# Kernel optimization log

Measured on AMD Instinct MI355X. Metric: run time of the kernel, lower is better.

## Reference

```python
import jax, jax.numpy as jnp
import numpy as np

NODE, PROJ, ATTN, NREL, NL = 1280, 2560, 256, 129, 4
B, L = 2, 1024
EPS = 1e-5


def _layernorm(x):
    m = jnp.mean(x, axis=-1, keepdims=True)
    v = jnp.var(x, axis=-1, keepdims=True)
    return (x - m) * jax.lax.rsqrt(v + EPS)


def _rope(x):
    # x: [B, L, 2, D]; rotary applied along the seq (L) axis, rotate-half convention
    d = x.shape[-1]
    freq = 10000.0 ** (-jnp.arange(0, d, 2, dtype=jnp.float32) / d)      # [d/2]
    ang = jnp.arange(x.shape[1], dtype=jnp.float32)[:, None] * freq      # [L, d/2]
    cos = jnp.concatenate([jnp.cos(ang), jnp.cos(ang)], -1)[:, None, :]  # [L,1,d]
    sin = jnp.concatenate([jnp.sin(ang), jnp.sin(ang)], -1)[:, None, :]
    x1, x2 = jnp.split(x, 2, axis=-1)
    return x * cos + jnp.concatenate([-x2, x1], -1) * sin


def _relpos_idx(n):
    i = np.arange(n)
    one = NREL // 2
    return jnp.asarray(np.clip(i[:, None] - i[None, :], -one, one) + one)  # [L,L] int32


def setup_inputs() -> dict:
    key = jax.random.key(0)
    ks = jax.random.split(key, 14)
    s = 0.02
    return {
        "node": jax.random.normal(ks[0], (B, L, NODE), jnp.float32),
        "qk_scaling": jax.random.uniform(ks[1], (B, L, 1), jnp.float32),
        "bias": jax.random.normal(ks[2], (B, 1, L), jnp.float32),
        "cond": jax.random.normal(ks[3], (B, NODE), jnp.float32),
        "w_gva": jax.random.normal(ks[4], (NL, NODE, 2 * PROJ + ATTN), jnp.float32) * s,
        "b_gva": jnp.zeros((NL, 2 * PROJ + ATTN), jnp.float32),
        "mhs_w": jax.random.normal(ks[5], (NL, 2, ATTN), jnp.float32) * s + 1.0,
        "mhs_b": jax.random.normal(ks[6], (NL, 2, ATTN), jnp.float32) * s,
        "relpos_emb": jax.random.normal(ks[7], (NL, NREL), jnp.float32) * s,
        "w_out": jax.random.normal(ks[8], (NL, PROJ, NODE), jnp.float32) * s,
        "b_out": jnp.zeros((NL, NODE), jnp.float32),
        "w_adaln": jax.random.normal(ks[9], (NL, NODE, 3 * NODE), jnp.float32) * s,
        "b_adaln": jnp.zeros((NL, 3 * NODE), jnp.float32),
        "subbatch_size": 256,
    }


def _forward(node, qk_scaling, bias, cond, w_gva, b_gva, mhs_w, mhs_b,
             relpos_emb, w_out, b_out, w_adaln, b_adaln, rel_idx):
    edge = None
    silu = jax.nn.silu
    for l in range(NL):
        # AdaLN conditioning: SiLU -> Linear(node, 3*node), chunk into gamma/beta/alpha [B,node]
        gba = silu(cond) @ w_adaln[l] + b_adaln[l]
        gamma, beta, alpha = jnp.split(gba, 3, axis=-1)
        shortcut = node
        x = _layernorm(node)
        x = x * (1.0 + gamma[:, None, :]) + beta[:, None, :]
        # GAU: joint gate/value/base projection + SiLU
        h = silu(x @ w_gva[l] + b_gva[l])                    # [B,L,2P+A]
        gates = h[..., :PROJ]
        values = h[..., PROJ:2 * PROJ]
        base = h[..., 2 * PROJ:]                             # [B,L,A]
        # multi-headed scaling (2 heads) + RoPE, unbind into q,k
        qk = base[..., None, :] * mhs_w[l] + mhs_b[l]        # [B,L,2,A]
        qk = _rope(qk)
        q, k = qk[..., 0, :], qk[..., 1, :]
        # attention with mask bias + relpos bias; query pre-scaled
        rel = relpos_emb[l][rel_idx]                         # [L,L]
        logits = jnp.einsum('bid,bjd->bij', q * qk_scaling, k) + (bias + rel)
        attn = jax.nn.softmax(logits, axis=-1)               # [B,L,L]
        out = jnp.einsum('bij,bjd->bid', attn, values)       # [B,L,P]
        edge = jnp.sum(attn, axis=-3)                        # sum-reduce over batch -> [L,L]
        out = out * gates
        out = out @ w_out[l] + b_out[l]
        node = out * (1.0 + alpha[:, None, :]) + shortcut
    return node, edge


def reference(node, qk_scaling, bias, cond, w_gva, b_gva, mhs_w, mhs_b,
              relpos_emb, w_out, b_out, w_adaln, b_adaln, subbatch_size):
    # subbatch_size only chunks queries for memory in the original; math-identical ignored
    rel_idx = _relpos_idx(node.shape[-2])
    return _forward(node, qk_scaling, bias, cond, w_gva, b_gva, mhs_w, mhs_b,
                    relpos_emb, w_out, b_out, w_adaln, b_adaln, rel_idx)
```

## Files before the change

### kernel.cpp

```cpp
#include <hip/hip_runtime.h>


typedef __bf16 bf16;
typedef __attribute__((ext_vector_type(8))) __bf16 bf16x8;
typedef __attribute__((ext_vector_type(4))) float f32x4;

#define NODE_D 1280
#define PROJ_D 2560
#define ATTN_D 256
#define HDIM 5376
#define LSEQ 1024
#define NTOK 2048

__device__ __forceinline__ void async_ld16(const void* gsrc, void* ldst) {
  __builtin_amdgcn_global_load_lds(
      (__attribute__((address_space(1))) void*)gsrc,
      (__attribute__((address_space(3))) void*)ldst, 16, 0, 0);
}

__device__ __forceinline__ float sigmoidf_fast(float x) {
  return 1.f / (1.f + __expf(-x));
}

template <int MODE>
__global__ __launch_bounds__(256, 3) void gemm_bt(
    const bf16* __restrict__ A, const bf16* __restrict__ Bt, int K,
    int lda, int ldb, void* __restrict__ C, int ldc,
    const void* __restrict__ E0, const void* __restrict__ E1,
    long zA, long zB, long zCb, long zE0b) {
  __shared__ __align__(16) bf16 As[128 * 64];
  __shared__ __align__(16) bf16 Bs[128 * 64];

  const int z = blockIdx.z;
  A += (size_t)zA * z;
  Bt += (size_t)zB * z;
  char* Cb = (char*)C + (size_t)zCb * z;
  const char* e0 = (const char*)E0 + (size_t)zE0b * z;

  const int rowBase = blockIdx.y * 128;
  const int colBase = blockIdx.x * 128;
  const int tid = threadIdx.x;
  const int lane = tid & 63;
  const int wv = tid >> 6;
  const int wrow = (wv >> 1) * 64;
  const int wcol = (wv & 1) * 64;
  const int fm = lane & 15;
  const int fq = lane >> 4;

  const bf16* Ablk = A + (size_t)rowBase * lda;
  const bf16* Bblk = Bt + (size_t)colBase * ldb;

  f32x4 zero = {0.f, 0.f, 0.f, 0.f};
  f32x4 acc[4][4];
#pragma unroll
  for (int i = 0; i < 4; i++)
#pragma unroll
    for (int j = 0; j < 4; j++) acc[i][j] = zero;

  for (int k0 = 0; k0 < K; k0 += 64) {
    __syncthreads();
#pragma unroll
    for (int i = 0; i < 4; i++) {
      const int slot = tid + i * 256;
      const int row = slot >> 3;
      const int u = (slot & 7) ^ (row & 7);
      bf16* dA = As + ((i * 256 + wv * 64) << 3);
      bf16* dB = Bs + ((i * 256 + wv * 64) << 3);
      async_ld16(Ablk + (size_t)row * lda + k0 + (u << 3), dA);
      async_ld16(Bblk + (size_t)row * ldb + k0 + (u << 3), dB);
    }
    __syncthreads();

#pragma unroll
    for (int s = 0; s < 2; s++) {
      bf16x8 aF[4], bF[4];
#pragma unroll
      for (int i = 0; i < 4; i++) {
        const int r = wrow + i * 16 + fm;
        aF[i] = *(const bf16x8*)(As + r * 64 +
                                 ((((s << 2) | fq) ^ (r & 7)) << 3));
      }
#pragma unroll
      for (int j = 0; j < 4; j++) {
        const int r = wcol + j * 16 + fm;
        bF[j] = *(const bf16x8*)(Bs + r * 64 +
                                 ((((s << 2) | fq) ^ (r & 7)) << 3));
      }
#pragma unroll
      for (int i = 0; i < 4; i++)
#pragma unroll
        for (int j = 0; j < 4; j++)
          acc[i][j] = __builtin_amdgcn_mfma_f32_16x16x32_bf16(
              aF[i], bF[j], acc[i][j], 0, 0, 0);
    }
  }

#pragma unroll
  for (int i = 0; i < 4; i++) {
#pragma unroll
    for (int t = 0; t < 4; t++) {
      const int r = rowBase + wrow + i * 16 + fq * 4 + t;
#pragma unroll
      for (int j = 0; j < 4; j++) {
        const int cc = colBase + wcol + j * 16 + fm;
        float v = acc[i][j][t];
        if constexpr (MODE == 0) {
          v += ((const float*)e0)[cc];
          v = v * sigmoidf_fast(v);
          ((bf16*)Cb)[(size_t)r * ldc + cc] = (bf16)v;
        } else if constexpr (MODE == 1) {
          v += ((const float*)e0)[cc];
          int d = r - cc;
          d = d < -64 ? -64 : (d > 64 ? 64 : d);
          v += ((const float*)E1)[d + 64];
          ((float*)Cb)[(size_t)r * ldc + cc] = v;
        } else if constexpr (MODE == 2) {
          float gt = (float)((const bf16*)e0)[(size_t)r * HDIM + cc];
          ((bf16*)Cb)[(size_t)r * ldc + cc] = (bf16)(v * gt);
        } else {
          ((float*)Cb)[(size_t)r * ldc + cc] = v;
        }
      }
    }
  }
}

__global__ void transpose_f2b(const float* __restrict__ in, bf16* __restrict__ out,
                              int ldin, int ldout) {
  __shared__ __align__(16) bf16 t[64][72];
  const int rb = blockIdx.y * 64, cb = blockIdx.x * 64;
  const int tx = threadIdx.x & 7, ty = threadIdx.x >> 3;
#pragma unroll
  for (int rr = 0; rr < 64; rr += 32) {
    const int r = ty + rr;
    const float4* p = (const float4*)&in[(size_t)(rb + r) * ldin + cb + tx * 8];
    float4 a = p[0], b = p[1];
    t[tx * 8 + 0][r] = (bf16)a.x; t[tx * 8 + 1][r] = (bf16)a.y;
    t[tx * 8 + 2][r] = (bf16)a.z; t[tx * 8 + 3][r] = (bf16)a.w;
    t[tx * 8 + 4][r] = (bf16)b.x; t[tx * 8 + 5][r] = (bf16)b.y;
    t[tx * 8 + 6][r] = (bf16)b.z; t[tx * 8 + 7][r] = (bf16)b.w;
  }
  __syncthreads();
#pragma unroll
  for (int rr = 0; rr < 64; rr += 32) {
    const int c = ty + rr;
    *(bf16x8*)&out[(size_t)(cb + c) * ldout + rb + tx * 8] =
        *(const bf16x8*)&t[c][tx * 8];
  }
}

__global__ void transpose_int(const bf16* __restrict__ in0, bf16* __restrict__ out0,
                              int ldin, int ldout, long zIn, long zOut) {
  __shared__ __align__(16) bf16 t[64][72];
  const bf16* in = in0 + (size_t)zIn * blockIdx.z;
  bf16* out = out0 + (size_t)zOut * blockIdx.z;
  const int rb = blockIdx.y * 64, cb = blockIdx.x * 64;
  const int tx = threadIdx.x & 7, ty = threadIdx.x >> 3;
#pragma unroll
  for (int rr = 0; rr < 64; rr += 32) {
    const int r = ty + rr;
    bf16x8 v = *(const bf16x8*)&in[(size_t)(rb + r) * ldin + cb + tx * 8];
#pragma unroll
    for (int e = 0; e < 8; e++) t[tx * 8 + e][r] = v[e];
  }
  __syncthreads();
#pragma unroll
  for (int rr = 0; rr < 64; rr += 32) {
    const int c = ty + rr;
    *(bf16x8*)&out[(size_t)(cb + c) * ldout + rb + tx * 8] =
        *(const bf16x8*)&t[c][tx * 8];
  }
}

__global__ void gba_init(const float* __restrict__ b_adaln,
                         float* __restrict__ gba) {
  const int i = blockIdx.x * 256 + threadIdx.x;
  if (i < 4 * 2 * 3840) {
    const int l = i / (2 * 3840);
    const int c = i % 3840;
    gba[i] = b_adaln[l * 3840 + c];
  }
}

__global__ void adaln_part(const float* __restrict__ cond,
                           const float* __restrict__ w_adaln,
                           float* __restrict__ gba) {
  __shared__ float sc[2 * NODE_D];
  __shared__ float red[2][2][128];
  const int l = blockIdx.y, z = blockIdx.z;
  const int cl = threadIdx.x & 127;
  const int col = blockIdx.x * 128 + cl;
  const int kg = threadIdx.x >> 7;
  for (int i = threadIdx.x; i < 2 * NODE_D; i += 256) {
    float v = cond[i];
    sc[i] = v * sigmoidf_fast(v);
  }
  __syncthreads();
  const float* w = w_adaln + (size_t)l * NODE_D * 3840;
  const int k0 = z * 160 + kg * 80;
  float a0 = 0.f, a1 = 0.f;
  for (int k = k0; k < k0 + 80; k++) {
    float wv = w[(size_t)k * 3840 + col];
    a0 += sc[k] * wv;
    a1 += sc[NODE_D + k] * wv;
  }
  red[kg][0][cl] = a0;
  red[kg][1][cl] = a1;
  __syncthreads();
  if (kg == 0) {
    a0 += red[1][0][cl];
    a1 += red[1][1][cl];
    atomicAdd(&gba[(size_t)(l * 2 + 0) * 3840 + col], a0);
    atomicAdd(&gba[(size_t)(l * 2 + 1) * 3840 + col], a1);
  }
}

__global__ void ln_mod_kernel(const float* __restrict__ nodef,
                              const float* __restrict__ gba_l,
                              bf16* __restrict__ xmod) {
  __shared__ float red[2][4];
  const int row = blockIdx.x, b = row >> 10, tt = threadIdx.x;
  const float* x = nodef + (size_t)row * NODE_D;
  float vals[5], s = 0.f, s2 = 0.f;
#pragma unroll
  for (int i = 0; i < 5; i++) {
    float v = x[tt + i * 256];
    vals[i] = v; s += v; s2 += v * v;
  }
#pragma unroll
  for (int off = 32; off >= 1; off >>= 1) {
    s += __shfl_down(s, off, 64);
    s2 += __shfl_down(s2, off, 64);
  }
  const int wv = tt >> 6, lane = tt & 63;
  if (lane == 0) { red[0][wv] = s; red[1][wv] = s2; }
  __syncthreads();
  s = red[0][0] + red[0][1] + red[0][2] + red[0][3];
  s2 = red[1][0] + red[1][1] + red[1][2] + red[1][3];
  const float mean = s * (1.f / NODE_D);
  const float var = s2 * (1.f / NODE_D) - mean * mean;
  const float inv = rsqrtf(var + 1e-5f);
  const float* gm = gba_l + b * 3840;
#pragma unroll
  for (int i = 0; i < 5; i++) {
    const int c = tt + i * 256;
    float v = (vals[i] - mean) * inv * (1.f + gm[c]) + gm[NODE_D + c];
    xmod[(size_t)row * NODE_D + c] = (bf16)v;
  }
}

template <bool LAST>
__global__ void res_ln_fuse(const float* __restrict__ p0,
                            const float* __restrict__ p1,
                            const float* __restrict__ b_out_l,
                            const float* __restrict__ gba_l,
                            const float* __restrict__ gba_next,
                            float* __restrict__ nodef,
                            bf16* __restrict__ xmod,
                            float* __restrict__ outNode) {
  __shared__ float red[2][4];
  const int row = blockIdx.x, b = row >> 10, tt = threadIdx.x;
  const float* a0 = p0 + (size_t)row * NODE_D;
  const float* a1 = p1 + (size_t)row * NODE_D;
  float* nd = nodef + (size_t)row * NODE_D;
  const float* al = gba_l + b * 3840 + 2560;
  float vals[5], s = 0.f, s2 = 0.f;
#pragma unroll
  for (int i = 0; i < 5; i++) {
    const int c = tt + i * 256;
    float delta = (a0[c] + a1[c] + b_out_l[c]) * (1.f + al[c]);
    float v = nd[c] + delta;
    if (LAST) {
      outNode[(size_t)row * NODE_D + c] = v;
    } else {
      nd[c] = v;
    }
    vals[i] = v; s += v; s2 += v * v;
  }
  if (!LAST) {
#pragma unroll
    for (int off = 32; off >= 1; off >>= 1) {
      s += __shfl_down(s, off, 64);
      s2 += __shfl_down(s2, off, 64);
    }
    const int wv = tt >> 6, lane = tt & 63;
    if (lane == 0) { red[0][wv] = s; red[1][wv] = s2; }
    __syncthreads();
    s = red[0][0] + red[0][1] + red[0][2] + red[0][3];
    s2 = red[1][0] + red[1][1] + red[1][2] + red[1][3];
    const float mean = s * (1.f / NODE_D);
    const float var = s2 * (1.f / NODE_D) - mean * mean;
    const float inv = rsqrtf(var + 1e-5f);
    const float* gm = gba_next + b * 3840;
#pragma unroll
    for (int i = 0; i < 5; i++) {
      const int c = tt + i * 256;
      float v = (vals[i] - mean) * inv * (1.f + gm[c]) + gm[NODE_D + c];
      xmod[(size_t)row * NODE_D + c] = (bf16)v;
    }
  }
}

__global__ void trig_init(float* __restrict__ tab) {
  const int pos = blockIdx.x;
  const int j = threadIdx.x;
  const float freq = __expf(-(float)j * 0.07195578415606392f);
  const float ang = (float)pos * freq;
  tab[(pos * 128 + j) * 2 + 0] = cosf(ang);
  tab[(pos * 128 + j) * 2 + 1] = sinf(ang);
}

__global__ void qk_rope_kernel(const bf16* __restrict__ h,
                               const float* __restrict__ mhs_w,
                               const float* __restrict__ mhs_b,
                               const float* __restrict__ qk_sc,
                               const float* __restrict__ trig,
                               bf16* __restrict__ q, bf16* __restrict__ k) {
  const int tok = blockIdx.x;
  const int pos = tok & (LSEQ - 1);
  const int d = threadIdx.x;
  const bf16* base = h + (size_t)tok * HDIM + 2 * PROJ_D;
  const int j = d & 127;
  const float2 cssn = ((const float2*)trig)[pos * 128 + j];
  const float cs = cssn.x, sn = cssn.y;
  const float bd = (float)base[d];
  const int pd = (d < 128) ? d + 128 : d - 128;
  const float bp = (float)base[pd];
  const float sgn = (d < 128) ? -1.f : 1.f;

  float v = bd * mhs_w[d] + mhs_b[d];
  float vp = bp * mhs_w[pd] + mhs_b[pd];
  float r0 = v * cs + sgn * vp * sn;
  q[(size_t)tok * ATTN_D + d] = (bf16)(r0 * qk_sc[tok]);

  float v1 = bd * mhs_w[ATTN_D + d] + mhs_b[ATTN_D + d];
  float v1p = bp * mhs_w[ATTN_D + pd] + mhs_b[ATTN_D + pd];
  float r1 = v1 * cs + sgn * v1p * sn;
  k[(size_t)tok * ATTN_D + d] = (bf16)r1;
}

__global__ void softmax_kernel(const float* __restrict__ S, bf16* __restrict__ P) {
  __shared__ float red[8];
  const size_t row = blockIdx.x;
  const float* s = S + row * LSEQ;
  const int tt = threadIdx.x, wv = tt >> 6, lane = tt & 63;
  float v[4];
  float m = -1e30f;
#pragma unroll
  for (int i = 0; i < 4; i++) {
    v[i] = s[tt + i * 256];
    m = fmaxf(m, v[i]);
  }
#pragma unroll
  for (int off = 32; off >= 1; off >>= 1) m = fmaxf(m, __shfl_down(m, off, 64));
  if (lane == 0) red[wv] = m;
  __syncthreads();
  m = fmaxf(fmaxf(red[0], red[1]), fmaxf(red[2], red[3]));
  float sum = 0.f;
#pragma unroll
  for (int i = 0; i < 4; i++) {
    v[i] = __expf(v[i] - m);
    sum += v[i];
  }
#pragma unroll
  for (int off = 32; off >= 1; off >>= 1) sum += __shfl_down(sum, off, 64);
  __syncthreads();
  if (lane == 0) red[4 + wv] = sum;
  __syncthreads();
  const float inv = 1.f / (red[4] + red[5] + red[6] + red[7]);
  bf16* p = P + row * LSEQ;
#pragma unroll
  for (int i = 0; i < 4; i++) p[tt + i * 256] = (bf16)(v[i] * inv);
}

__global__ void copy_f32(const float* __restrict__ in, float* __restrict__ out,
                         int n) {
  int i = (blockIdx.x * 256 + threadIdx.x) * 4;
  if (i < n) *(float4*)(out + i) = *(const float4*)(in + i);
}

__global__ void edge_kernel(const bf16* __restrict__ P, float* __restrict__ out) {
  const int idx = (blockIdx.x * 256 + threadIdx.x) * 4;
#pragma unroll
  for (int i = 0; i < 4; i++)
    out[idx + i] = (float)P[idx + i] + (float)P[1048576 + idx + i];
}

extern "C" void kernel_launch(void* const* d_in, const int* in_sizes, int n_in,
                              void* d_out, int out_size, void* d_ws, size_t ws_size,
                              hipStream_t stream) {
  const float* node_in = (const float*)d_in[0];
  const float* qk_sc   = (const float*)d_in[1];
  const float* bias    = (const float*)d_in[2];
  const float* cond    = (const float*)d_in[3];
  const float* w_gva   = (const float*)d_in[4];
  const float* b_gva   = (const float*)d_in[5];
  const float* mhs_w   = (const float*)d_in[6];
  const float* mhs_b   = (const float*)d_in[7];
  const float* relpos  = (const float*)d_in[8];
  const float* w_out   = (const float*)d_in[9];
  const float* b_out   = (const float*)d_in[10];
  const float* w_adaln = (const float*)d_in[11];
  const float* b_adaln = (const float*)d_in[12];
  (void)in_sizes; (void)n_in; (void)out_size; (void)ws_size;

  char* wsp = (char*)d_ws;
  auto alloc = [&](size_t bytes) {
    char* p = wsp;
    wsp += (bytes + 255) & ~(size_t)255;
    return p;
  };
  float* nodef = (float*)alloc((size_t)NTOK * NODE_D * 4);
  float* gba   = (float*)alloc((size_t)8 * 3840 * 4);
  bf16* xmod   = (bf16*)alloc((size_t)NTOK * NODE_D * 2);
  bf16* h      = (bf16*)alloc((size_t)NTOK * HDIM * 2);
  bf16* q      = (bf16*)alloc((size_t)NTOK * ATTN_D * 2);
  bf16* kk     = (bf16*)alloc((size_t)NTOK * ATTN_D * 2);
  bf16* Vt     = (bf16*)alloc((size_t)2 * PROJ_D * LSEQ * 2);
  bf16* wT     = (bf16*)alloc((size_t)HDIM * NODE_D * 2);
  float* S     = (float*)wT;
  bf16* P      = (bf16*)alloc((size_t)2 * LSEQ * LSEQ * 2);
  bf16* po     = (bf16*)alloc((size_t)NTOK * PROJ_D * 2);
  float* Pp    = (float*)alloc((size_t)2 * NTOK * NODE_D * 4);
  float* trig  = (float*)alloc((size_t)LSEQ * 128 * 2 * 4);

  float* outNode = (float*)d_out;
  float* outEdge = outNode + (size_t)NTOK * NODE_D;

  copy_f32<<<2560, 256, 0, stream>>>(node_in, nodef, NTOK * NODE_D);
  trig_init<<<1024, 128, 0, stream>>>(trig);
  gba_init<<<120, 256, 0, stream>>>(b_adaln, gba);
  adaln_part<<<dim3(30, 4, 8), 256, 0, stream>>>(cond, w_adaln, gba);
  ln_mod_kernel<<<2048, 256, 0, stream>>>(nodef, gba, xmod);

  for (int l = 0; l < 4; ++l) {
    transpose_f2b<<<dim3(84, 20), 256, 0, stream>>>(
        w_gva + (size_t)l * NODE_D * HDIM, wT, HDIM, NODE_D);
    gemm_bt<0><<<dim3(42, 16, 1), 256, 0, stream>>>(
        xmod, wT, NODE_D, NODE_D, NODE_D, h, HDIM,
        b_gva + (size_t)l * HDIM, nullptr, 0, 0, 0, 0);

    qk_rope_kernel<<<2048, 256, 0, stream>>>(h, mhs_w + l * 2 * ATTN_D,
                                             mhs_b + l * 2 * ATTN_D, qk_sc,
                                             trig, q, kk);

    transpose_int<<<dim3(40, 16, 2), 256, 0, stream>>>(
        h + PROJ_D, Vt, HDIM, LSEQ, (long)LSEQ * HDIM, (long)PROJ_D * LSEQ);

    gemm_bt<1><<<dim3(8, 8, 2), 256, 0, stream>>>(
        q, kk, ATTN_D, ATTN_D, ATTN_D, S, LSEQ,
        bias, relpos + l * 129,
        (long)LSEQ * ATTN_D, (long)LSEQ * ATTN_D, (long)LSEQ * LSEQ * 4,
        (long)LSEQ * 4);

    softmax_kernel<<<2048, 256, 0, stream>>>(S, P);
    if (l == 3) edge_kernel<<<1024, 256, 0, stream>>>(P, outEdge);

    gemm_bt<2><<<dim3(20, 8, 2), 256, 0, stream>>>(
        P, Vt, LSEQ, LSEQ, LSEQ, po, PROJ_D,
        h, nullptr,
        (long)LSEQ * LSEQ, (long)PROJ_D * LSEQ, (long)LSEQ * PROJ_D * 2,
        (long)LSEQ * HDIM * 2);

    transpose_f2b<<<dim3(20, 40), 256, 0, stream>>>(
        w_out + (size_t)l * PROJ_D * NODE_D, wT, NODE_D, PROJ_D);
    gemm_bt<4><<<dim3(10, 16, 2), 256, 0, stream>>>(
        po, wT, 1280, PROJ_D, PROJ_D, Pp, NODE_D,
        nullptr, nullptr,
        1280, 1280, (long)NTOK * NODE_D * 4, 0);

    if (l < 3) {
      res_ln_fuse<false><<<2048, 256, 0, stream>>>(
          Pp, Pp + (size_t)NTOK * NODE_D, b_out + (size_t)l * NODE_D,
          gba + l * 2 * 3840, gba + (l + 1) * 2 * 3840, nodef, xmod, nullptr);
    } else {
      res_ln_fuse<true><<<2048, 256, 0, stream>>>(
          Pp, Pp + (size_t)NTOK * NODE_D, b_out + (size_t)l * NODE_D,
          gba + l * 2 * 3840, nullptr, nodef, nullptr, outNode);
    }
  }
}
```

Before: 793.6 us.

## Batch weight transposes upfront, drop node copy, and swizzle GEMM block order

All four layers' w_gva and w_out transposes are batched into two launches before the layer loop, with a dedicated buffer per layer, and S gets its own allocation instead of aliasing the weight buffer. The initial node copy kernel is removed: the first LN and the first residual read node_in directly. The GEMM also remaps block indices into eight interleaved groups to change L2 locality across workgroups. This trades more workspace memory for fewer launches and a different block-to-tile mapping.

After: 811.1 us. +2.2%, slower.

```diff
diff --git a/kernel.cpp b/kernel.cpp
--- a/kernel.cpp
+++ b/kernel.cpp
@@ -37,8 +37,21 @@
   char* Cb = (char*)C + (size_t)zCb * z;
   const char* e0 = (const char*)E0 + (size_t)zE0b * z;
 
-  const int rowBase = blockIdx.y * 128;
-  const int colBase = blockIdx.x * 128;
+  int bx = blockIdx.x, by = blockIdx.y;
+  {
+    const int gx = gridDim.x, gy = gridDim.y;
+    const int n = gx * gy;
+    if ((n & 7) == 0) {
+      const int cpx = n >> 3;
+      const int p = by * gx + bx;
+      const int lg = (p & 7) * cpx + (p >> 3);
+      bx = lg / gy;
+      by = lg % gy;
+    }
+  }
+
+  const int rowBase = by * 128;
+  const int colBase = bx * 128;
   const int tid = threadIdx.x;
   const int lane = tid & 63;
   const int wv = tid >> 6;
@@ -125,9 +138,12 @@
   }
 }
 
-__global__ void transpose_f2b(const float* __restrict__ in, bf16* __restrict__ out,
-                              int ldin, int ldout) {
+__global__ void transpose_f2b(const float* __restrict__ in0,
+                              bf16* __restrict__ out0, int ldin, int ldout,
+                              long zIn, long zOut) {
   __shared__ __align__(16) bf16 t[64][72];
+  const float* in = in0 + (size_t)zIn * blockIdx.z;
+  bf16* out = out0 + (size_t)zOut * blockIdx.z;
   const int rb = blockIdx.y * 64, cb = blockIdx.x * 64;
   const int tx = threadIdx.x & 7, ty = threadIdx.x >> 3;
 #pragma unroll
@@ -215,12 +231,12 @@
   }
 }
 
-__global__ void ln_mod_kernel(const float* __restrict__ nodef,
+__global__ void ln_mod_kernel(const float* __restrict__ xin,
                               const float* __restrict__ gba_l,
                               bf16* __restrict__ xmod) {
   __shared__ float red[2][4];
   const int row = blockIdx.x, b = row >> 10, tt = threadIdx.x;
-  const float* x = nodef + (size_t)row * NODE_D;
+  const float* x = xin + (size_t)row * NODE_D;
   float vals[5], s = 0.f, s2 = 0.f;
 #pragma unroll
   for (int i = 0; i < 5; i++) {
@@ -255,6 +271,7 @@
                             const float* __restrict__ b_out_l,
                             const float* __restrict__ gba_l,
                             const float* __restrict__ gba_next,
+                            const float* __restrict__ resid,
                             float* __restrict__ nodef,
                             bf16* __restrict__ xmod,
                             float* __restrict__ outNode) {
@@ -262,18 +279,18 @@
   const int row = blockIdx.x, b = row >> 10, tt = threadIdx.x;
   const float* a0 = p0 + (size_t)row * NODE_D;
   const float* a1 = p1 + (size_t)row * NODE_D;
-  float* nd = nodef + (size_t)row * NODE_D;
+  const float* rs = resid + (size_t)row * NODE_D;
   const float* al = gba_l + b * 3840 + 2560;
   float vals[5], s = 0.f, s2 = 0.f;
 #pragma unroll
   for (int i = 0; i < 5; i++) {
     const int c = tt + i * 256;
     float delta = (a0[c] + a1[c] + b_out_l[c]) * (1.f + al[c]);
-    float v = nd[c] + delta;
+    float v = rs[c] + delta;
     if (LAST) {
       outNode[(size_t)row * NODE_D + c] = v;
     } else {
-      nd[c] = v;
+      nodef[(size_t)row * NODE_D + c] = v;
     }
     vals[i] = v; s += v; s2 += v * v;
   }
@@ -373,12 +390,6 @@
   for (int i = 0; i < 4; i++) p[tt + i * 256] = (bf16)(v[i] * inv);
 }
 
-__global__ void copy_f32(const float* __restrict__ in, float* __restrict__ out,
-                         int n) {
-  int i = (blockIdx.x * 256 + threadIdx.x) * 4;
-  if (i < n) *(float4*)(out + i) = *(const float4*)(in + i);
-}
-
 __global__ void edge_kernel(const bf16* __restrict__ P, float* __restrict__ out) {
   const int idx = (blockIdx.x * 256 + threadIdx.x) * 4;
 #pragma unroll
@@ -417,8 +428,9 @@
   bf16* q      = (bf16*)alloc((size_t)NTOK * ATTN_D * 2);
   bf16* kk     = (bf16*)alloc((size_t)NTOK * ATTN_D * 2);
   bf16* Vt     = (bf16*)alloc((size_t)2 * PROJ_D * LSEQ * 2);
-  bf16* wT     = (bf16*)alloc((size_t)HDIM * NODE_D * 2);
-  float* S     = (float*)wT;
+  bf16* wTg    = (bf16*)alloc((size_t)4 * HDIM * NODE_D * 2);
+  bf16* wTo    = (bf16*)alloc((size_t)4 * NODE_D * PROJ_D * 2);
+  float* S     = (float*)alloc((size_t)2 * LSEQ * LSEQ * 4);
   bf16* P      = (bf16*)alloc((size_t)2 * LSEQ * LSEQ * 2);
   bf16* po     = (bf16*)alloc((size_t)NTOK * PROJ_D * 2);
   float* Pp    = (float*)alloc((size_t)2 * NTOK * NODE_D * 4);
@@ -427,17 +439,18 @@
   float* outNode = (float*)d_out;
   float* outEdge = outNode + (size_t)NTOK * NODE_D;
 
-  copy_f32<<<2560, 256, 0, stream>>>(node_in, nodef, NTOK * NODE_D);
   trig_init<<<1024, 128, 0, stream>>>(trig);
   gba_init<<<120, 256, 0, stream>>>(b_adaln, gba);
   adaln_part<<<dim3(30, 4, 8), 256, 0, stream>>>(cond, w_adaln, gba);
-  ln_mod_kernel<<<2048, 256, 0, stream>>>(nodef, gba, xmod);
+  ln_mod_kernel<<<2048, 256, 0, stream>>>(node_in, gba, xmod);
+  transpose_f2b<<<dim3(84, 20, 4), 256, 0, stream>>>(
+      w_gva, wTg, HDIM, NODE_D, (long)NODE_D * HDIM, (long)HDIM * NODE_D);
+  transpose_f2b<<<dim3(20, 40, 4), 256, 0, stream>>>(
+      w_out, wTo, NODE_D, PROJ_D, (long)PROJ_D * NODE_D, (long)NODE_D * PROJ_D);
 
   for (int l = 0; l < 4; ++l) {
-    transpose_f2b<<<dim3(84, 20), 256, 0, stream>>>(
-        w_gva + (size_t)l * NODE_D * HDIM, wT, HDIM, NODE_D);
     gemm_bt<0><<<dim3(42, 16, 1), 256, 0, stream>>>(
-        xmod, wT, NODE_D, NODE_D, NODE_D, h, HDIM,
+        xmod, wTg + (size_t)l * HDIM * NODE_D, NODE_D, NODE_D, NODE_D, h, HDIM,
         b_gva + (size_t)l * HDIM, nullptr, 0, 0, 0, 0);
 
     qk_rope_kernel<<<2048, 256, 0, stream>>>(h, mhs_w + l * 2 * ATTN_D,
@@ -462,21 +475,21 @@
         (long)LSEQ * LSEQ, (long)PROJ_D * LSEQ, (long)LSEQ * PROJ_D * 2,
         (long)LSEQ * HDIM * 2);
 
-    transpose_f2b<<<dim3(20, 40), 256, 0, stream>>>(
-        w_out + (size_t)l * PROJ_D * NODE_D, wT, NODE_D, PROJ_D);
     gemm_bt<4><<<dim3(10, 16, 2), 256, 0, stream>>>(
-        po, wT, 1280, PROJ_D, PROJ_D, Pp, NODE_D,
+        po, wTo + (size_t)l * NODE_D * PROJ_D, 1280, PROJ_D, PROJ_D, Pp, NODE_D,
         nullptr, nullptr,
         1280, 1280, (long)NTOK * NODE_D * 4, 0);
 
+    const float* resid = (l == 0) ? node_in : nodef;
     if (l < 3) {
       res_ln_fuse<false><<<2048, 256, 0, stream>>>(
           Pp, Pp + (size_t)NTOK * NODE_D, b_out + (size_t)l * NODE_D,
-          gba + l * 2 * 3840, gba + (l + 1) * 2 * 3840, nodef, xmod, nullptr);
+          gba + l * 2 * 3840, gba + (l + 1) * 2 * 3840, resid, nodef, xmod,
+          nullptr);
     } else {
       res_ln_fuse<true><<<2048, 256, 0, stream>>>(
           Pp, Pp + (size_t)NTOK * NODE_D, b_out + (size_t)l * NODE_D,
-          gba + l * 2 * 3840, nullptr, nodef, nullptr, outNode);
-    }
-  }
-}
+          gba + l * 2 * 3840, nullptr, resid, nodef, nullptr, outNode);
+    }
+  }
+}
```
